# Kernel optimization log

Measured on AMD Instinct MI355X. Metric: run time of the kernel, lower is better.

## Reference

```python
import math
import jax
import jax.numpy as jnp
import numpy as np

B, N, NPOINT, K = 8, 2048, 512, 16
CIN = 64
MLP = [64, 128, 256]
M_W = 8    # PAConv weight-bank size
HID = 16   # scorenet hidden width
GEOM = 10  # 3 rel-xyz + 1 dist + 3 norm + 3 angles


def setup_inputs():
    key = jax.random.key(0)
    ks = jax.random.split(key, 40)
    inp = {}
    inp['xyz'] = jax.random.normal(ks[0], (B, 3, N), jnp.float32)
    inp['norm'] = jax.random.normal(ks[1], (B, 3, N), jnp.float32)
    inp['X_axis'] = jax.random.normal(ks[2], (B, 3, N), jnp.float32)
    inp['Y_axis'] = jax.random.normal(ks[3], (B, 3, N), jnp.float32)
    inp['points'] = jax.random.normal(ks[4], (B, CIN, N), jnp.float32) * 0.5
    cin = CIN
    ki = 5
    for l, cout in enumerate(MLP):
        inp['w1_%d' % l] = jax.random.normal(ks[ki], (HID, GEOM), jnp.float32) / np.sqrt(GEOM); ki += 1
        inp['b1_%d' % l] = jnp.zeros((HID,), jnp.float32)
        inp['w2_%d' % l] = jax.random.normal(ks[ki], (M_W, HID), jnp.float32) / np.sqrt(HID); ki += 1
        inp['b2_%d' % l] = jnp.zeros((M_W,), jnp.float32)
        inp['bank_%d' % l] = jax.random.normal(ks[ki], (M_W, cin, cout), jnp.float32) / np.sqrt(cin); ki += 1
        if l < len(MLP) - 1:
            inp['gamma_%d' % l] = jnp.ones((cout,), jnp.float32)
            inp['beta_%d' % l] = jnp.zeros((cout,), jnp.float32)
        cin = cout
    return inp


def _group(t, idx):
    # t: (B, C, N), idx: (B, ...) int -> (B, C, ...)
    return jax.vmap(lambda p, i: p[:, i])(t, idx)


def _fps(xyz_t, npoint):
    # xyz_t: (B, N, 3) -> (B, npoint) int32; standard iterative FPS starting at index 0
    b, n, _ = xyz_t.shape
    def body(i, c):
        idxs, dists, far = c
        idxs = idxs.at[:, i].set(far)
        centroid = jnp.take_along_axis(xyz_t, far[:, None, None], axis=1)  # (B,1,3)
        d = jnp.sum((xyz_t - centroid) ** 2, axis=-1)
        dists = jnp.minimum(dists, d)
        return idxs, dists, jnp.argmax(dists, axis=-1).astype(jnp.int32)
    idxs = jnp.zeros((b, npoint), jnp.int32)
    dists = jnp.full((b, n), 1e10, xyz_t.dtype)
    far = jnp.zeros((b,), jnp.int32)
    idxs, _, _ = jax.lax.fori_loop(0, npoint, body, (idxs, dists, far))
    return idxs


def _sqdist(a, b):
    # a: (B, P, 3), b: (B, N, 3) -> (B, P, N)
    return (jnp.sum(a ** 2, -1)[:, :, None] + jnp.sum(b ** 2, -1)[:, None, :]
            - 2.0 * jnp.einsum('bpc,bnc->bpn', a, b))


def _angles(gxyz, gn, gX, gY):
    # all (B, 3, P, K) -> (B, 3, P, K); normalized angles to z(norm)/x/y frame axes
    nn = jnp.linalg.norm(gxyz, axis=1)
    def ang(v):
        c = jnp.sum(gxyz * v, axis=1) / (nn * jnp.linalg.norm(v, axis=1) + 1e-8)
        return jnp.arccos(jnp.clip(c, -1.0, 1.0)) / math.pi
    return jnp.stack([ang(gn), ang(gX), ang(gY)], axis=1)


def _paconv(geom, feats, w1, b1, w2, b2, bank, gamma=None, beta=None, act=True):
    # ScoreNet over geometric channels -> softmax scores over M weight matrices
    h = jax.nn.relu(jnp.einsum('hg,bgpk->bhpk', w1, geom) + b1[None, :, None, None])
    s = jax.nn.softmax(jnp.einsum('mh,bhpk->bmpk', w2, h) + b2[None, :, None, None], axis=1)
    out = jnp.einsum('bcpk,mco,bmpk->bopk', feats, bank, s)
    if gamma is not None:
        mu = out.mean(axis=(0, 2, 3), keepdims=True)
        var = out.var(axis=(0, 2, 3), keepdims=True)
        out = (out - mu) / jnp.sqrt(var + 1e-5) * gamma[None, :, None, None] + beta[None, :, None, None]
    return jax.nn.relu(out) if act else out


def reference(xyz, norm, X_axis, Y_axis, points,
              w1_0, b1_0, w2_0, b2_0, bank_0, gamma_0, beta_0,
              w1_1, b1_1, w2_1, b2_1, bank_1, gamma_1, beta_1,
              w1_2, b1_2, w2_2, b2_2, bank_2):
    xyz_t = jnp.transpose(xyz, (0, 2, 1))           # (B,N,3)
    fidx = _fps(xyz_t, NPOINT)                      # (B,NPOINT)
    new_xyz = _group(xyz, fidx)                     # (B,3,NPOINT)
    sq = _sqdist(jnp.transpose(new_xyz, (0, 2, 1)), xyz_t)  # (B,NPOINT,N)
    idx = jax.lax.top_k(-sq, K)[1]                  # (B,NPOINT,K) ascending distance
    grouped_xyz = _group(xyz, idx) - new_xyz[:, :, :, None]  # (B,3,NPOINT,K)
    dist = jnp.sqrt(jnp.sum(grouped_xyz ** 2, axis=1) + 1e-10)  # (B,NPOINT,K)
    dmin = dist.min(axis=2, keepdims=True)
    dist = (dist - dmin) / (dist.max(axis=2, keepdims=True) - dmin + 1e-10)
    new_points = _group(points, idx)                # (B,CIN,NPOINT,K)
    grouped_norm = _group(norm, idx)
    grouped_X = _group(X_axis, idx)
    grouped_Y = _group(Y_axis, idx)
    grouped_angles = _angles(grouped_xyz, grouped_norm, grouped_X, grouped_Y)
    new_norm = grouped_norm[:, :, :, 0]
    new_X = grouped_X[:, :, :, 0]
    new_Y = grouped_Y[:, :, :, 0]
    geom = jnp.concatenate([grouped_xyz, dist[:, None], grouped_norm, grouped_angles], axis=1)  # (B,10,NPOINT,K)
    new_points = _paconv(geom, new_points, w1_0, b1_0, w2_0, b2_0, bank_0, gamma_0, beta_0, act=True)
    new_points = _paconv(geom, new_points, w1_1, b1_1, w2_1, b2_1, bank_1, gamma_1, beta_1, act=True)
    new_points = _paconv(geom, new_points, w1_2, b1_2, w2_2, b2_2, bank_2, None, None, act=False)
    new_points = jnp.max(new_points, axis=3)        # (B,MLP[-1],NPOINT)
    return (new_xyz, new_norm, new_X, new_Y, new_points)
```

## Files before the change

### kernel.cpp

```cpp
#include <hip/hip_runtime.h>
#include <math.h>

#define NBATCH 8
#define NPTS   2048
#define NPOINT 512
#define KNB    16
#define NROWS  (NBATCH*NPOINT*KNB)

typedef unsigned short ushort_t;
typedef unsigned int   uint_t;
typedef unsigned long long ull_t;
typedef __attribute__((ext_vector_type(8))) short  short8;
typedef __attribute__((ext_vector_type(4))) float  f32x4;

#define B0_OFF 0
#define B1_OFF 32768
#define B2_OFF 98304
#define BT_TOT 360448

#define LDS_BARRIER() asm volatile("s_waitcnt lgkmcnt(0)\n\ts_barrier" ::: "memory")

__device__ __align__(16) int      g_fidx[NBATCH * NPOINT];
__device__ __align__(16) int      g_knn [NROWS];
__device__ __align__(16) float    g_sums[1024];
__device__ __align__(16) float    g_pT  [NBATCH * NPTS * 64];
__device__ __align__(16) float    g_S   [(size_t)3 * NROWS * 8];
__device__ __align__(16) float    g_act1[(size_t)NROWS * 64];
__device__ __align__(16) float    g_act2[(size_t)NROWS * 128];
__device__ __align__(16) ushort_t g_bankF[BT_TOT];

__device__ __forceinline__ ushort_t f2bf(float f) {
    uint_t u = __float_as_uint(f);
    return (ushort_t)((u + 0x7FFFu + ((u >> 16) & 1u)) >> 16);
}

template<int CTRL>
__device__ __forceinline__ ull_t dpp_u64(ull_t k) {
    int lo = (int)(uint_t)k;
    int hi = (int)(uint_t)(k >> 32);
    int slo = __builtin_amdgcn_update_dpp(0, lo, CTRL, 0xF, 0xF, true);
    int shi = __builtin_amdgcn_update_dpp(0, hi, CTRL, 0xF, 0xF, true);
    return ((ull_t)(uint_t)shi << 32) | (uint_t)slo;
}

__device__ __forceinline__ ull_t dpp_max_u64(ull_t key) {
    { ull_t s = dpp_u64<0x111>(key); if (s > key) key = s; }
    { ull_t s = dpp_u64<0x112>(key); if (s > key) key = s; }
    { ull_t s = dpp_u64<0x114>(key); if (s > key) key = s; }
    { ull_t s = dpp_u64<0x118>(key); if (s > key) key = s; }
    { ull_t s = dpp_u64<0x142>(key); if (s > key) key = s; }
    { ull_t s = dpp_u64<0x143>(key); if (s > key) key = s; }
    return key;
}

template<int COUT>
__device__ __forceinline__ void bank_frag(const float* __restrict__ bank,
                                          ushort_t* __restrict__ dst, int e) {
    const int j = e & 7;
    const int lane = (e >> 3) & 63;
    const int rem = e >> 9;
    constexpr int NTL = COUT / 16;
    const int nt = rem % NTL;
    const int kc = rem / NTL;
    const int q = lane >> 4, nlo = lane & 15;
    const int k = kc * 32 + q * 8 + j;
    const int n = nt * 16 + nlo;
    dst[e] = f2bf(bank[(size_t)k * COUT + n]);
}

__global__ __launch_bounds__(512) void front_kernel(const float* __restrict__ xyz,
                                                    const float* __restrict__ points,
                                                    const float* __restrict__ bank0,
                                                    const float* __restrict__ bank1,
                                                    const float* __restrict__ bank2) {
    __shared__ float smem[3 * NPTS];
    __shared__ ull_t s_key[2][8];
    const int bid = blockIdx.x;
    const int t = threadIdx.x;

    if (bid >= NBATCH) {
        if (bid < NBATCH + 256) {
            float (*tile)[65] = reinterpret_cast<float(*)[65]>(smem);
            const int blk = bid - NBATCH;
            const int b = blk >> 5;
            const int n0 = (blk & 31) * 64;
            const int lane = t & 63, q = t >> 6;
            #pragma unroll
            for (int i = 0; i < 8; ++i) {
                int c = q * 8 + i;
                tile[c][lane] = points[(b * 64 + c) * NPTS + n0 + lane];
            }
            __syncthreads();
            #pragma unroll
            for (int i = 0; i < 8; ++i) {
                int n = q * 8 + i;
                g_pT[(size_t)(b * NPTS + n0 + n) * 64 + lane] = tile[lane][n];
            }
        } else if (bid == NBATCH + 256) {
            g_sums[t] = 0.0f;
            g_sums[512 + t] = 0.0f;
        } else {
            const int e = (bid - (NBATCH + 257)) * 512 + t;
            if (e < 32768) {
                bank_frag<64>(bank0, g_bankF + B0_OFF, e);
            } else if (e < 98304) {
                bank_frag<128>(bank1, g_bankF + B1_OFF, e - 32768);
            } else {
                bank_frag<256>(bank2, g_bankF + B2_OFF, e - 98304);
            }
        }
        return;
    }

    {
        #pragma clang fp contract(off)
        const int b = bid;
        const int lane = t & 63, w8 = t >> 6;
        const float* xb = xyz + b * 3 * NPTS;
        float* s_x = smem;
        float* s_y = smem + NPTS;
        float* s_z = smem + 2 * NPTS;
        float x[4], y[4], z[4], d[4];
        #pragma unroll
        for (int j = 0; j < 4; ++j) {
            int p = j * 512 + t;
            float vx = xb[p], vy = xb[NPTS + p], vz = xb[2*NPTS + p];
            x[j] = vx; y[j] = vy; z[j] = vz;
            s_x[p] = vx; s_y[p] = vy; s_z[p] = vz;
            d[j] = 1e10f;
        }
        __syncthreads();
        int far = 0;
        for (int i = 0; i < NPOINT; ++i) {
            if (t == 0) g_fidx[b * NPOINT + i] = far;
            float cx = s_x[far], cy = s_y[far], cz = s_z[far];
            float best = -1.0f; int bi = 0;
            #pragma unroll
            for (int j = 0; j < 4; ++j) {
                float dx = x[j] - cx;
                float dy = y[j] - cy;
                float dz = z[j] - cz;
                float dd = dx*dx + dy*dy;
                dd = dd + dz*dz;
                float dn = fminf(d[j], dd);
                d[j] = dn;
                if (dn > best) { best = dn; bi = j * 512 + t; }
            }
            ull_t key = (((ull_t)__float_as_uint(best)) << 32) | (uint_t)(~bi);
            key = dpp_max_u64(key);
            uint_t wlo = (uint_t)__builtin_amdgcn_readlane((int)(uint_t)key, 63);
            uint_t whi = (uint_t)__builtin_amdgcn_readlane((int)(uint_t)(key >> 32), 63);
            if (lane == 0) s_key[i & 1][w8] = ((ull_t)whi << 32) | wlo;
            __syncthreads();
            const ull_t* kb = s_key[i & 1];
            ull_t k0 = kb[0], k1 = kb[1], k2 = kb[2], k3 = kb[3];
            ull_t k4 = kb[4], k5 = kb[5], k6 = kb[6], k7 = kb[7];
            if (k1 > k0) k0 = k1;
            if (k3 > k2) k2 = k3;
            if (k5 > k4) k4 = k5;
            if (k7 > k6) k6 = k7;
            if (k2 > k0) k0 = k2;
            if (k6 > k4) k4 = k6;
            if (k4 > k0) k0 = k4;
            far = (int)(~(uint_t)k0) & (NPTS - 1);
        }
    }
}

__global__ __launch_bounds__(256) void knn_score_kernel(
    const float* __restrict__ xyz, const float* __restrict__ nrm,
    const float* __restrict__ Xa, const float* __restrict__ Ya,
    const float* __restrict__ w1_0, const float* __restrict__ b1_0,
    const float* __restrict__ w2_0, const float* __restrict__ b2_0,
    const float* __restrict__ w1_1, const float* __restrict__ b1_1,
    const float* __restrict__ w2_1, const float* __restrict__ b2_1,
    const float* __restrict__ w1_2, const float* __restrict__ b1_2,
    const float* __restrict__ w2_2, const float* __restrict__ b2_2) {
    __shared__ float w1s[3][16][10];
    __shared__ float b1s[3][16];
    __shared__ float w2s[3][8][16];
    __shared__ float b2s[3][8];
    const int t = threadIdx.x;
    {
        const float* w1p[3] = {w1_0, w1_1, w1_2};
        const float* b1p[3] = {b1_0, b1_1, b1_2};
        const float* w2p[3] = {w2_0, w2_1, w2_2};
        const float* b2p[3] = {b2_0, b2_1, b2_2};
        #pragma unroll
        for (int l = 0; l < 3; ++l) {
            if (t < 160) w1s[l][t / 10][t % 10] = w1p[l][t];
            if (t < 16)  b1s[l][t] = b1p[l][t];
            if (t < 128) w2s[l][t / 16][t % 16] = w2p[l][t];
            if (t < 8)   b2s[l][t] = b2p[l][t];
        }
    }
    __syncthreads();

    const int wave = blockIdx.x * 4 + (t >> 6);
    const int lane = t & 63;
    const int b = wave >> 9;
    const float* xb = xyz + b * 3 * NPTS;
    const int fi = g_fidx[wave] & (NPTS - 1);
    int nmine = 0;

    {
        #pragma clang fp contract(off)
        float ax = xb[fi];
        float ay = xb[NPTS + fi];
        float az = xb[2*NPTS + fi];
        float sa = ax*ax + ay*ay; sa = sa + az*az;
        float d[32];
        #pragma unroll
        for (int j = 0; j < 32; ++j) {
            int pp = j * 64 + lane;
            float bx = xb[pp];
            float by = xb[NPTS + pp];
            float bz = xb[2*NPTS + pp];
            float sb = bx*bx + by*by; sb = sb + bz*bz;
            float dot = ax*bx + ay*by; dot = dot + az*bz;
            float t1 = sa + sb;
            float t2 = 2.0f * dot;
            d[j] = t1 - t2;
        }
        for (int r = 0; r < KNB; ++r) {
            float best = 1e30f; int bi = 0x7fffffff;
            #pragma unroll
            for (int j = 0; j < 32; ++j) {
                if (d[j] < best) { best = d[j]; bi = j * 64 + lane; }
            }
            uint_t ub = __float_as_uint(best);
            ub = (ub & 0x80000000u) ? ~ub : (ub | 0x80000000u);
            ull_t key = ((ull_t)(~ub) << 32) | (uint_t)(~bi);
            key = dpp_max_u64(key);
            uint_t wlo = (uint_t)__builtin_amdgcn_readlane((int)(uint_t)key, 63);
            bi = (int)(~wlo) & (NPTS - 1);
            if (lane == 0) g_knn[wave * KNB + r] = bi;
            if (lane == r) nmine = bi;
            int rl = bi & 63, rs = bi >> 6;
            if (lane == rl) {
                #pragma unroll
                for (int j = 0; j < 32; ++j) if (j == rs) d[j] = 1e30f;
            }
        }
    }

    if (lane < 16) {
        const int row = wave * KNB + lane;
        const int n = nmine & (NPTS - 1);
        const float* nb = nrm + b * 3 * NPTS;
        const float* Xb = Xa  + b * 3 * NPTS;
        const float* Yb = Ya  + b * 3 * NPTS;
        float gx, gy, gz, sq, draw, nnv;
        {
            #pragma clang fp contract(off)
            gx = xb[n]        - xb[fi];
            gy = xb[NPTS + n] - xb[NPTS + fi];
            gz = xb[2*NPTS+n] - xb[2*NPTS+fi];
            sq = gx*gx + gy*gy;
            sq = sq + gz*gz;
            draw = sqrtf(sq + 1e-10f);
            nnv = sqrtf(sq);
        }
        float dmin = draw, dmax = draw;
        #pragma unroll
        for (int m = 1; m < 16; m <<= 1) {
            dmin = fminf(dmin, __shfl_xor(dmin, m, 16));
            dmax = fmaxf(dmax, __shfl_xor(dmax, m, 16));
        }
        float dist;
        {
            #pragma clang fp contract(off)
            dist = (draw - dmin) / ((dmax - dmin) + 1e-10f);
        }
        float nx = nb[n], ny = nb[NPTS+n], nz = nb[2*NPTS+n];
        float Xx = Xb[n], Xy = Xb[NPTS+n], Xz = Xb[2*NPTS+n];
        float Yx = Yb[n], Yy = Yb[NPTS+n], Yz = Yb[2*NPTS+n];
        float g[10];
        g[0]=gx; g[1]=gy; g[2]=gz; g[3]=dist; g[4]=nx; g[5]=ny; g[6]=nz;
        {
            float vs[3][3] = {{nx,ny,nz},{Xx,Xy,Xz},{Yx,Yy,Yz}};
            #pragma unroll
            for (int a = 0; a < 3; ++a) {
                float vx=vs[a][0], vy=vs[a][1], vz=vs[a][2];
                float dot, nv;
                {
                    #pragma clang fp contract(off)
                    dot = gx*vx + gy*vy; dot = dot + gz*vz;
                    float s2 = vx*vx + vy*vy; s2 = s2 + vz*vz;
                    nv = sqrtf(s2);
                }
                float cc = dot / (nnv * nv + 1e-8f);
                cc = fminf(1.0f, fmaxf(-1.0f, cc));
                g[7+a] = acosf(cc) / 3.14159274101257324f;
            }
        }
        #pragma unroll
        for (int l = 0; l < 3; ++l) {
            float h[16];
            #pragma unroll
            for (int i = 0; i < 16; ++i) {
                float a = b1s[l][i];
                #pragma unroll
                for (int j = 0; j < 10; ++j) a += w1s[l][i][j] * g[j];
                h[i] = fmaxf(a, 0.0f);
            }
            float e[8]; float mx = -1e30f;
            #pragma unroll
            for (int m = 0; m < 8; ++m) {
                float a = b2s[l][m];
                #pragma unroll
                for (int j = 0; j < 16; ++j) a += w2s[l][m][j] * h[j];
                e[m] = a; mx = fmaxf(mx, a);
            }
            float sum = 0.0f;
            #pragma unroll
            for (int m = 0; m < 8; ++m) { e[m] = expf(e[m] - mx); sum += e[m]; }
            #pragma unroll
            for (int m = 0; m < 8; ++m)
                g_S[(size_t)l * NROWS * 8 + (size_t)row * 8 + m] = e[m] / sum;
        }
    }
}

template<int LAYER, int CIN, int COUT>
__global__ __launch_bounds__(256) void gemm_kernel(const float* __restrict__ gamma,
                                                   const float* __restrict__ beta,
                                                   float* __restrict__ dout,
                                                   const float* __restrict__ xyz,
                                                   const float* __restrict__ nrm,
                                                   const float* __restrict__ Xa,
                                                   const float* __restrict__ Ya) {
    if constexpr (LAYER == 0) {
        if (blockIdx.x >= 1024) {
            const int g = (blockIdx.x - 1024) * 256 + threadIdx.x;
            const int b = g / NPOINT, p = g % NPOINT;
            const int fi = g_fidx[g] & (NPTS - 1);
            const int n0 = g_knn[g * KNB] & (NPTS - 1);
            #pragma unroll
            for (int a = 0; a < 3; ++a) {
                dout[            (b*3 + a) * NPOINT + p] = xyz[(b*3 + a) * NPTS + fi];
                dout[12288 +     (b*3 + a) * NPOINT + p] = nrm[(b*3 + a) * NPTS + n0];
                dout[24576 +     (b*3 + a) * NPOINT + p] = Xa [(b*3 + a) * NPTS + n0];
                dout[36864 +     (b*3 + a) * NPOINT + p] = Ya [(b*3 + a) * NPTS + n0];
            }
            return;
        }
    }

    const float* __restrict__ A = (LAYER == 0) ? g_pT : (LAYER == 1) ? g_act1 : g_act2;
    float* __restrict__ O = (LAYER == 0) ? g_act1 : (LAYER == 1) ? g_act2 : dout;
    constexpr int NTT = COUT / 16;
    constexpr int NTW = NTT / 4;
    constexpr int CCM = CIN / 32;
    constexpr int BOFF = (LAYER == 0) ? B0_OFF : (LAYER == 1) ? B1_OFF : B2_OFF;
    __shared__ ushort_t As[2][64][36];
    __shared__ float s_scale[(LAYER >= 1) ? CIN : 1];
    __shared__ float s_shift[(LAYER >= 1) ? CIN : 1];
    __shared__ float s_rs[(LAYER < 2) ? COUT : 1];
    __shared__ float s_rss[(LAYER < 2) ? COUT : 1];

    const int t = threadIdx.x;
    const int lane = t & 63, w = t >> 6;
    const int q = lane >> 4, nlo = lane & 15;
    const int row0 = blockIdx.x * 64;
    const int arow_i = t >> 2, acg = t & 3;

    if constexpr (LAYER >= 1) {
        const float* sb = (LAYER == 1) ? g_sums : (g_sums + 256);
        if (t < CIN) {
            float mu  = sb[t] * (1.0f / 65536.0f);
            float var = sb[CIN + t] * (1.0f / 65536.0f) - mu * mu;
            var = fmaxf(var, 0.0f);
            float sc = gamma[t] / sqrtf(var + 1e-5f);
            s_scale[t] = sc;
            s_shift[t] = beta[t] - mu * sc;
        }
        __syncthreads();
    }

    size_t arow;
    if (LAYER == 0) {
        const int row = row0 + arow_i;
        const int b = row >> 13;
        const int n = g_knn[row] & (NPTS - 1);
        arow = (size_t)(b * NPTS + n) * 64;
    } else {
        arow = (size_t)(row0 + arow_i) * CIN;
    }
    const float* Sbase = g_S + (size_t)LAYER * NROWS * 8 + (size_t)(row0 + arow_i) * 8;

    float svv[8];
    #pragma unroll
    for (int m = 0; m < 8; ++m) svv[m] = Sbase[m];

    f32x4 acc[4][NTW];
    #pragma unroll
    for (int mi = 0; mi < 4; ++mi)
        #pragma unroll
        for (int ni = 0; ni < NTW; ++ni) acc[mi][ni] = (f32x4){0.f, 0.f, 0.f, 0.f};

    const ushort_t* fbase = g_bankF + BOFF + lane * 8;

    union FragU { uint4 u4; uint2 u2[2]; short8 s; };
    FragU B[2][NTW];
    #pragma unroll
    for (int ni = 0; ni < NTW; ++ni)
        B[0][ni].u4 = *reinterpret_cast<const uint4*>(fbase + (size_t)(w * NTW + ni) * 512);

    float vraw[8], vnext[8];
    {
        const float* ap = A + arow + acg * 8;
        float4 fa = *reinterpret_cast<const float4*>(ap);
        float4 fb = *reinterpret_cast<const float4*>(ap + 4);
        vraw[0]=fa.x; vraw[1]=fa.y; vraw[2]=fa.z; vraw[3]=fa.w;
        vraw[4]=fb.x; vraw[5]=fb.y; vraw[6]=fb.z; vraw[7]=fb.w;
    }

    int par = 0;
    for (int cc = 0; cc < CCM; ++cc) {
        float v[8];
        #pragma unroll
        for (int j = 0; j < 8; ++j) {
            if constexpr (LAYER >= 1) {
                const int c = cc * 32 + acg * 8 + j;
                v[j] = fmaxf(vraw[j] * s_scale[c] + s_shift[c], 0.f);
            } else {
                v[j] = vraw[j];
            }
        }
        #pragma unroll
        for (int m = 0; m < 8; ++m) {
            {
                const float sv = svv[m];
                uint_t* dst = reinterpret_cast<uint_t*>(&As[par][arow_i][acg * 8]);
                #pragma unroll
                for (int j = 0; j < 8; j += 2)
                    dst[j >> 1] = (uint_t)f2bf(sv * v[j]) | ((uint_t)f2bf(sv * v[j+1]) << 16);
            }
            if (m == 0) {
                const int ccn = (cc + 1 < CCM) ? cc + 1 : cc;
                const float* ap = A + arow + ccn * 32 + acg * 8;
                float4 fa = *reinterpret_cast<const float4*>(ap);
                float4 fb = *reinterpret_cast<const float4*>(ap + 4);
                vnext[0]=fa.x; vnext[1]=fa.y; vnext[2]=fa.z; vnext[3]=fa.w;
                vnext[4]=fb.x; vnext[5]=fb.y; vnext[6]=fb.z; vnext[7]=fb.w;
            }
            {
                const int kcn = (m < 7) ? ((m + 1) * CCM + cc)
                                        : ((cc + 1 < CCM) ? (cc + 1) : 0);
                #pragma unroll
                for (int ni = 0; ni < NTW; ++ni)
                    B[(m + 1) & 1][ni].u4 = *reinterpret_cast<const uint4*>(
                        fbase + (size_t)(kcn * NTT + w * NTW + ni) * 512);
            }
            LDS_BARRIER();
            FragU af[4];
            #pragma unroll
            for (int mi = 0; mi < 4; ++mi) {
                af[mi].u2[0] = *reinterpret_cast<const uint2*>(&As[par][mi*16 + nlo][q*8]);
                af[mi].u2[1] = *reinterpret_cast<const uint2*>(&As[par][mi*16 + nlo][q*8 + 4]);
            }
            #pragma unroll
            for (int ni = 0; ni < NTW; ++ni)
                #pragma unroll
                for (int mi = 0; mi < 4; ++mi)
                    acc[mi][ni] = __builtin_amdgcn_mfma_f32_16x16x32_bf16(
                        af[mi].s, B[m & 1][ni].s, acc[mi][ni], 0, 0, 0);
            par ^= 1;
        }
        #pragma unroll
        for (int j = 0; j < 8; ++j) vraw[j] = vnext[j];
    }

    if constexpr (LAYER == 2) {
        const int bp0 = row0 >> 4;
        #pragma unroll
        for (int mi = 0; mi < 4; ++mi) {
            const int bp = bp0 + mi;
            const int b = bp >> 9, p = bp & 511;
            #pragma unroll
            for (int ni = 0; ni < NTW; ++ni) {
                float mv = fmaxf(fmaxf(acc[mi][ni][0], acc[mi][ni][1]),
                                 fmaxf(acc[mi][ni][2], acc[mi][ni][3]));
                mv = fmaxf(mv, __shfl_xor(mv, 16));
                mv = fmaxf(mv, __shfl_xor(mv, 32));
                if (lane < 16) {
                    const int col = w * 64 + ni * 16 + nlo;
                    O[(size_t)(b * 256 + col) * NPOINT + p] = mv;
                }
            }
        }
    } else {
        #pragma unroll
        for (int mi = 0; mi < 4; ++mi)
            #pragma unroll
            for (int ni = 0; ni < NTW; ++ni)
                #pragma unroll
                for (int r2 = 0; r2 < 4; ++r2)
                    O[(size_t)(row0 + mi*16 + q*4 + r2) * COUT + w*NTW*16 + ni*16 + nlo] = acc[mi][ni][r2];
        #pragma unroll
        for (int ni = 0; ni < NTW; ++ni) {
            float s = 0.f, ss = 0.f;
            #pragma unroll
            for (int mi = 0; mi < 4; ++mi) {
                #pragma unroll
                for (int r2 = 0; r2 < 4; ++r2) {
                    float x = acc[mi][ni][r2];
                    s += x; ss += x * x;
                }
            }
            s  += __shfl_xor(s, 16);  s  += __shfl_xor(s, 32);
            ss += __shfl_xor(ss, 16); ss += __shfl_xor(ss, 32);
            if (q == 0) {
                const int c = w * NTW * 16 + ni * 16 + nlo;
                s_rs[c] = s;
                s_rss[c] = ss;
            }
        }
        __syncthreads();
        if (t < COUT) {
            float* sb = (LAYER == 0) ? g_sums : (g_sums + 256);
            atomicAdd(&sb[t], s_rs[t]);
            atomicAdd(&sb[COUT + t], s_rss[t]);
        }
    }
}

extern "C" void kernel_launch(void* const* d_in, const int* in_sizes, int n_in,
                              void* d_out, int out_size, void* d_ws, size_t ws_size,
                              hipStream_t stream) {
    const float* xyz    = (const float*)d_in[0];
    const float* nrm    = (const float*)d_in[1];
    const float* Xa     = (const float*)d_in[2];
    const float* Ya     = (const float*)d_in[3];
    const float* points = (const float*)d_in[4];
    const float* w1_0 = (const float*)d_in[5];  const float* b1_0 = (const float*)d_in[6];
    const float* w2_0 = (const float*)d_in[7];  const float* b2_0 = (const float*)d_in[8];
    const float* bank0 = (const float*)d_in[9];
    const float* g0 = (const float*)d_in[10];   const float* be0 = (const float*)d_in[11];
    const float* w1_1 = (const float*)d_in[12]; const float* b1_1 = (const float*)d_in[13];
    const float* w2_1 = (const float*)d_in[14]; const float* b2_1 = (const float*)d_in[15];
    const float* bank1 = (const float*)d_in[16];
    const float* g1 = (const float*)d_in[17];   const float* be1 = (const float*)d_in[18];
    const float* w1_2 = (const float*)d_in[19]; const float* b1_2 = (const float*)d_in[20];
    const float* w2_2 = (const float*)d_in[21]; const float* b2_2 = (const float*)d_in[22];
    const float* bank2 = (const float*)d_in[23];
    float* out = (float*)d_out;
    (void)d_ws; (void)ws_size; (void)in_sizes; (void)n_in; (void)out_size;

    front_kernel<<<969, 512, 0, stream>>>(xyz, points, bank0, bank1, bank2);
    knn_score_kernel<<<1024, 256, 0, stream>>>(xyz, nrm, Xa, Ya,
                                               w1_0, b1_0, w2_0, b2_0,
                                               w1_1, b1_1, w2_1, b2_1,
                                               w1_2, b1_2, w2_2, b2_2);
    gemm_kernel<0, 64, 64><<<1040, 256, 0, stream>>>(nullptr, nullptr, out, xyz, nrm, Xa, Ya);
    gemm_kernel<1, 64, 128><<<1024, 256, 0, stream>>>(g0, be0, nullptr, nullptr, nullptr, nullptr, nullptr);
    gemm_kernel<2, 128, 256><<<1024, 256, 0, stream>>>(g1, be1, out + 49152, nullptr, nullptr, nullptr, nullptr);
}
```

Baseline: 507.5 us.

## Shrink FPS block to 4 waves and reduce argmax via 32-bit DPP max

```diff
diff --git a/kernel.cpp b/kernel.cpp
--- a/kernel.cpp
+++ b/kernel.cpp
@@ -51,6 +51,21 @@
     { ull_t s = dpp_u64<0x142>(key); if (s > key) key = s; }
     { ull_t s = dpp_u64<0x143>(key); if (s > key) key = s; }
     return key;
+}
+
+template<int CTRL>
+__device__ __forceinline__ uint_t dpp_u32(uint_t v) {
+    return (uint_t)__builtin_amdgcn_update_dpp(0, (int)v, CTRL, 0xF, 0xF, true);
+}
+
+__device__ __forceinline__ uint_t dpp_max_u32(uint_t v) {
+    { uint_t s = dpp_u32<0x111>(v); if (s > v) v = s; }
+    { uint_t s = dpp_u32<0x112>(v); if (s > v) v = s; }
+    { uint_t s = dpp_u32<0x114>(v); if (s > v) v = s; }
+    { uint_t s = dpp_u32<0x118>(v); if (s > v) v = s; }
+    { uint_t s = dpp_u32<0x142>(v); if (s > v) v = s; }
+    { uint_t s = dpp_u32<0x143>(v); if (s > v) v = s; }
+    return v;
 }
 
 template<int COUT>
@@ -68,13 +83,13 @@
     dst[e] = f2bf(bank[(size_t)k * COUT + n]);
 }
 
-__global__ __launch_bounds__(512) void front_kernel(const float* __restrict__ xyz,
+__global__ __launch_bounds__(256) void front_kernel(const float* __restrict__ xyz,
                                                     const float* __restrict__ points,
                                                     const float* __restrict__ bank0,
                                                     const float* __restrict__ bank1,
                                                     const float* __restrict__ bank2) {
     __shared__ float smem[3 * NPTS];
-    __shared__ ull_t s_key[2][8];
+    __shared__ ull_t s_key[2][4];
     const int bid = blockIdx.x;
     const int t = threadIdx.x;
 
@@ -86,21 +101,23 @@
             const int n0 = (blk & 31) * 64;
             const int lane = t & 63, q = t >> 6;
             #pragma unroll
-            for (int i = 0; i < 8; ++i) {
-                int c = q * 8 + i;
+            for (int i = 0; i < 16; ++i) {
+                int c = q * 16 + i;
                 tile[c][lane] = points[(b * 64 + c) * NPTS + n0 + lane];
             }
             __syncthreads();
             #pragma unroll
-            for (int i = 0; i < 8; ++i) {
-                int n = q * 8 + i;
+            for (int i = 0; i < 16; ++i) {
+                int n = q * 16 + i;
                 g_pT[(size_t)(b * NPTS + n0 + n) * 64 + lane] = tile[lane][n];
             }
         } else if (bid == NBATCH + 256) {
             g_sums[t] = 0.0f;
+            g_sums[256 + t] = 0.0f;
             g_sums[512 + t] = 0.0f;
+            g_sums[768 + t] = 0.0f;
         } else {
-            const int e = (bid - (NBATCH + 257)) * 512 + t;
+            const int e = (bid - (NBATCH + 257)) * 256 + t;
             if (e < 32768) {
                 bank_frag<64>(bank0, g_bankF + B0_OFF, e);
             } else if (e < 98304) {
@@ -115,28 +132,42 @@
     {
         #pragma clang fp contract(off)
         const int b = bid;
-        const int lane = t & 63, w8 = t >> 6;
+        const int lane = t & 63, w = t >> 6;
         const float* xb = xyz + b * 3 * NPTS;
         float* s_x = smem;
         float* s_y = smem + NPTS;
         float* s_z = smem + 2 * NPTS;
-        float x[4], y[4], z[4], d[4];
-        #pragma unroll
-        for (int j = 0; j < 4; ++j) {
-            int p = j * 512 + t;
-            float vx = xb[p], vy = xb[NPTS + p], vz = xb[2*NPTS + p];
-            x[j] = vx; y[j] = vy; z[j] = vz;
-            s_x[p] = vx; s_y[p] = vy; s_z[p] = vz;
-            d[j] = 1e10f;
+        float x[8], y[8], z[8], d[8];
+        {
+            const float4* xp = reinterpret_cast<const float4*>(xb + t * 8);
+            const float4* yp = reinterpret_cast<const float4*>(xb + NPTS + t * 8);
+            const float4* zp = reinterpret_cast<const float4*>(xb + 2 * NPTS + t * 8);
+            float4 a0 = xp[0], a1 = xp[1];
+            float4 b0 = yp[0], b1 = yp[1];
+            float4 c0 = zp[0], c1 = zp[1];
+            x[0]=a0.x; x[1]=a0.y; x[2]=a0.z; x[3]=a0.w;
+            x[4]=a1.x; x[5]=a1.y; x[6]=a1.z; x[7]=a1.w;
+            y[0]=b0.x; y[1]=b0.y; y[2]=b0.z; y[3]=b0.w;
+            y[4]=b1.x; y[5]=b1.y; y[6]=b1.z; y[7]=b1.w;
+            z[0]=c0.x; z[1]=c0.y; z[2]=c0.z; z[3]=c0.w;
+            z[4]=c1.x; z[5]=c1.y; z[6]=c1.z; z[7]=c1.w;
+            *reinterpret_cast<float4*>(s_x + t * 8)     = a0;
+            *reinterpret_cast<float4*>(s_x + t * 8 + 4) = a1;
+            *reinterpret_cast<float4*>(s_y + t * 8)     = b0;
+            *reinterpret_cast<float4*>(s_y + t * 8 + 4) = b1;
+            *reinterpret_cast<float4*>(s_z + t * 8)     = c0;
+            *reinterpret_cast<float4*>(s_z + t * 8 + 4) = c1;
+            #pragma unroll
+            for (int j = 0; j < 8; ++j) d[j] = 1e10f;
         }
         __syncthreads();
         int far = 0;
         for (int i = 0; i < NPOINT; ++i) {
             if (t == 0) g_fidx[b * NPOINT + i] = far;
             float cx = s_x[far], cy = s_y[far], cz = s_z[far];
-            float best = -1.0f; int bi = 0;
-            #pragma unroll
-            for (int j = 0; j < 4; ++j) {
+            uint_t bb = 0u;
+            #pragma unroll
+            for (int j = 0; j < 8; ++j) {
                 float dx = x[j] - cx;
                 float dy = y[j] - cy;
                 float dz = z[j] - cz;
@@ -144,24 +175,26 @@
                 dd = dd + dz*dz;
                 float dn = fminf(d[j], dd);
                 d[j] = dn;
-                if (dn > best) { best = dn; bi = j * 512 + t; }
-            }
-            ull_t key = (((ull_t)__float_as_uint(best)) << 32) | (uint_t)(~bi);
-            key = dpp_max_u64(key);
-            uint_t wlo = (uint_t)__builtin_amdgcn_readlane((int)(uint_t)key, 63);
-            uint_t whi = (uint_t)__builtin_amdgcn_readlane((int)(uint_t)(key >> 32), 63);
-            if (lane == 0) s_key[i & 1][w8] = ((ull_t)whi << 32) | wlo;
-            __syncthreads();
+                uint_t ub = __float_as_uint(dn);
+                bb = (ub > bb) ? ub : bb;
+            }
+            uint_t wm = dpp_max_u32(bb);
+            uint_t wbits = (uint_t)__builtin_amdgcn_readlane((int)wm, 63);
+            int li = 8;
+            #pragma unroll
+            for (int j = 7; j >= 0; --j)
+                li = (__float_as_uint(d[j]) == wbits) ? j : li;
+            ull_t mk = __ballot(li < 8);
+            int fl = __ffsll((unsigned long long)mk) - 1;
+            int wj = __builtin_amdgcn_readlane(li, fl);
+            int wp = ((w << 6) + fl) * 8 + wj;
+            if (lane == 0) s_key[i & 1][w] = ((ull_t)wbits << 32) | (uint_t)(~wp);
+            LDS_BARRIER();
             const ull_t* kb = s_key[i & 1];
             ull_t k0 = kb[0], k1 = kb[1], k2 = kb[2], k3 = kb[3];
-            ull_t k4 = kb[4], k5 = kb[5], k6 = kb[6], k7 = kb[7];
             if (k1 > k0) k0 = k1;
             if (k3 > k2) k2 = k3;
-            if (k5 > k4) k4 = k5;
-            if (k7 > k6) k6 = k7;
             if (k2 > k0) k0 = k2;
-            if (k6 > k4) k4 = k6;
-            if (k4 > k0) k0 = k4;
             far = (int)(~(uint_t)k0) & (NPTS - 1);
         }
     }
@@ -548,7 +581,7 @@
     float* out = (float*)d_out;
     (void)d_ws; (void)ws_size; (void)in_sizes; (void)n_in; (void)out_size;
 
-    front_kernel<<<969, 512, 0, stream>>>(xyz, points, bank0, bank1, bank2);
+    front_kernel<<<1673, 256, 0, stream>>>(xyz, points, bank0, bank1, bank2);
     knn_score_kernel<<<1024, 256, 0, stream>>>(xyz, nrm, Xa, Ya,
                                                w1_0, b1_0, w2_0, b2_0,
                                                w1_1, b1_1, w2_1, b2_1,
```

Measured after the change: 473.4 us. 6.7% less time.

## Restructure FPS loop: 256 threads, packed-f32 distances, broadcast winner coords via LDS

Applied to the files above, without the earlier changes.

```diff
diff --git a/kernel.cpp b/kernel.cpp
--- a/kernel.cpp
+++ b/kernel.cpp
@@ -12,6 +12,7 @@
 typedef unsigned long long ull_t;
 typedef __attribute__((ext_vector_type(8))) short  short8;
 typedef __attribute__((ext_vector_type(4))) float  f32x4;
+typedef __attribute__((ext_vector_type(2))) float  f32x2;
 
 #define B0_OFF 0
 #define B1_OFF 32768
@@ -32,6 +33,13 @@
 __device__ __forceinline__ ushort_t f2bf(float f) {
     uint_t u = __float_as_uint(f);
     return (ushort_t)((u + 0x7FFFu + ((u >> 16) & 1u)) >> 16);
+}
+
+__device__ __forceinline__ f32x2 pk_add(f32x2 a, f32x2 b) {
+    f32x2 r; asm("v_pk_add_f32 %0, %1, %2" : "=v"(r) : "v"(a), "v"(b)); return r;
+}
+__device__ __forceinline__ f32x2 pk_mul(f32x2 a, f32x2 b) {
+    f32x2 r; asm("v_pk_mul_f32 %0, %1, %2" : "=v"(r) : "v"(a), "v"(b)); return r;
 }
 
 template<int CTRL>
@@ -68,13 +76,13 @@
     dst[e] = f2bf(bank[(size_t)k * COUT + n]);
 }
 
-__global__ __launch_bounds__(512) void front_kernel(const float* __restrict__ xyz,
+__global__ __launch_bounds__(256) void front_kernel(const float* __restrict__ xyz,
                                                     const float* __restrict__ points,
                                                     const float* __restrict__ bank0,
                                                     const float* __restrict__ bank1,
                                                     const float* __restrict__ bank2) {
     __shared__ float smem[3 * NPTS];
-    __shared__ ull_t s_key[2][8];
+    __shared__ uint4 s_slot[2][4];
     const int bid = blockIdx.x;
     const int t = threadIdx.x;
 
@@ -86,21 +94,23 @@
             const int n0 = (blk & 31) * 64;
             const int lane = t & 63, q = t >> 6;
             #pragma unroll
-            for (int i = 0; i < 8; ++i) {
-                int c = q * 8 + i;
+            for (int i = 0; i < 16; ++i) {
+                int c = q * 16 + i;
                 tile[c][lane] = points[(b * 64 + c) * NPTS + n0 + lane];
             }
             __syncthreads();
             #pragma unroll
-            for (int i = 0; i < 8; ++i) {
-                int n = q * 8 + i;
+            for (int i = 0; i < 16; ++i) {
+                int n = q * 16 + i;
                 g_pT[(size_t)(b * NPTS + n0 + n) * 64 + lane] = tile[lane][n];
             }
         } else if (bid == NBATCH + 256) {
             g_sums[t] = 0.0f;
+            g_sums[256 + t] = 0.0f;
             g_sums[512 + t] = 0.0f;
+            g_sums[768 + t] = 0.0f;
         } else {
-            const int e = (bid - (NBATCH + 257)) * 512 + t;
+            const int e = (bid - (NBATCH + 257)) * 256 + t;
             if (e < 32768) {
                 bank_frag<64>(bank0, g_bankF + B0_OFF, e);
             } else if (e < 98304) {
@@ -115,54 +125,94 @@
     {
         #pragma clang fp contract(off)
         const int b = bid;
-        const int lane = t & 63, w8 = t >> 6;
+        const int w = t >> 6;
         const float* xb = xyz + b * 3 * NPTS;
-        float* s_x = smem;
-        float* s_y = smem + NPTS;
-        float* s_z = smem + 2 * NPTS;
-        float x[4], y[4], z[4], d[4];
-        #pragma unroll
-        for (int j = 0; j < 4; ++j) {
-            int p = j * 512 + t;
-            float vx = xb[p], vy = xb[NPTS + p], vz = xb[2*NPTS + p];
-            x[j] = vx; y[j] = vy; z[j] = vz;
-            s_x[p] = vx; s_y[p] = vy; s_z[p] = vz;
-            d[j] = 1e10f;
-        }
-        __syncthreads();
-        int far = 0;
-        for (int i = 0; i < NPOINT; ++i) {
-            if (t == 0) g_fidx[b * NPOINT + i] = far;
-            float cx = s_x[far], cy = s_y[far], cz = s_z[far];
-            float best = -1.0f; int bi = 0;
-            #pragma unroll
-            for (int j = 0; j < 4; ++j) {
-                float dx = x[j] - cx;
-                float dy = y[j] - cy;
-                float dz = z[j] - cz;
-                float dd = dx*dx + dy*dy;
-                dd = dd + dz*dz;
-                float dn = fminf(d[j], dd);
-                d[j] = dn;
-                if (dn > best) { best = dn; bi = j * 512 + t; }
-            }
-            ull_t key = (((ull_t)__float_as_uint(best)) << 32) | (uint_t)(~bi);
+        f32x2 xp[4], yp[4], zp[4];
+        float d[8];
+        {
+            const float4* xq = reinterpret_cast<const float4*>(xb + t * 8);
+            const float4* yq = reinterpret_cast<const float4*>(xb + NPTS + t * 8);
+            const float4* zq = reinterpret_cast<const float4*>(xb + 2 * NPTS + t * 8);
+            float4 a0 = xq[0], a1 = xq[1];
+            float4 b0 = yq[0], b1 = yq[1];
+            float4 c0 = zq[0], c1 = zq[1];
+            xp[0] = (f32x2){a0.x, a0.y}; xp[1] = (f32x2){a0.z, a0.w};
+            xp[2] = (f32x2){a1.x, a1.y}; xp[3] = (f32x2){a1.z, a1.w};
+            yp[0] = (f32x2){b0.x, b0.y}; yp[1] = (f32x2){b0.z, b0.w};
+            yp[2] = (f32x2){b1.x, b1.y}; yp[3] = (f32x2){b1.z, b1.w};
+            zp[0] = (f32x2){c0.x, c0.y}; zp[1] = (f32x2){c0.z, c0.w};
+            zp[2] = (f32x2){c1.x, c1.y}; zp[3] = (f32x2){c1.z, c1.w};
+            #pragma unroll
+            for (int j = 0; j < 8; ++j) d[j] = 1e10f;
+        }
+        float cx = xb[0], cy = xb[NPTS], cz = xb[2 * NPTS];
+        if (t == 0) g_fidx[b * NPOINT] = 0;
+
+        for (int i = 0; i < NPOINT - 1; ++i) {
+            const float ncx = -cx, ncy = -cy, ncz = -cz;
+            const f32x2 ncxp = (f32x2){ncx, ncx};
+            const f32x2 ncyp = (f32x2){ncy, ncy};
+            const f32x2 nczp = (f32x2){ncz, ncz};
+            #pragma unroll
+            for (int a = 0; a < 4; ++a) {
+                f32x2 dx = pk_add(xp[a], ncxp);
+                f32x2 dy = pk_add(yp[a], ncyp);
+                f32x2 dz = pk_add(zp[a], nczp);
+                f32x2 px = pk_mul(dx, dx);
+                f32x2 py = pk_mul(dy, dy);
+                f32x2 s  = pk_add(px, py);
+                f32x2 pz = pk_mul(dz, dz);
+                s = pk_add(s, pz);
+                d[2*a]   = fminf(d[2*a],   s[0]);
+                d[2*a+1] = fminf(d[2*a+1], s[1]);
+            }
+            float bb = fmaxf(fmaxf(fmaxf(d[0], d[1]), fmaxf(d[2], d[3])),
+                             fmaxf(fmaxf(d[4], d[5]), fmaxf(d[6], d[7])));
+            const uint_t lb = __float_as_uint(bb);
+            int li = 7;
+            #pragma unroll
+            for (int j = 6; j >= 0; --j)
+                li = (__float_as_uint(d[j]) == lb) ? j : li;
+            ull_t key = ((ull_t)lb << 32) | (uint_t)(~(t * 8 + li));
             key = dpp_max_u64(key);
-            uint_t wlo = (uint_t)__builtin_amdgcn_readlane((int)(uint_t)key, 63);
-            uint_t whi = (uint_t)__builtin_amdgcn_readlane((int)(uint_t)(key >> 32), 63);
-            if (lane == 0) s_key[i & 1][w8] = ((ull_t)whi << 32) | wlo;
-            __syncthreads();
-            const ull_t* kb = s_key[i & 1];
-            ull_t k0 = kb[0], k1 = kb[1], k2 = kb[2], k3 = kb[3];
-            ull_t k4 = kb[4], k5 = kb[5], k6 = kb[6], k7 = kb[7];
-            if (k1 > k0) k0 = k1;
-            if (k3 > k2) k2 = k3;
-            if (k5 > k4) k4 = k5;
-            if (k7 > k6) k6 = k7;
-            if (k2 > k0) k0 = k2;
-            if (k6 > k4) k4 = k6;
-            if (k4 > k0) k0 = k4;
-            far = (int)(~(uint_t)k0) & (NPTS - 1);
+            const uint_t klo = (uint_t)__builtin_amdgcn_readlane((int)(uint_t)key, 63);
+            const uint_t khi = (uint_t)__builtin_amdgcn_readlane((int)(uint_t)(key >> 32), 63);
+            const int wp = (int)(~klo) & (NPTS - 1);
+            if (t == (wp >> 3)) {
+                const int jw = wp & 7;
+                float cxc = xp[0][0], cyc = yp[0][0], czc = zp[0][0];
+                #pragma unroll
+                for (int j = 1; j < 8; ++j) {
+                    const bool m = (jw == j);
+                    cxc = m ? xp[j >> 1][j & 1] : cxc;
+                    cyc = m ? yp[j >> 1][j & 1] : cyc;
+                    czc = m ? zp[j >> 1][j & 1] : czc;
+                }
+                uint4 sl;
+                sl.x = khi;
+                sl.y = __float_as_uint(cxc);
+                sl.z = __float_as_uint(cyc);
+                sl.w = __float_as_uint(czc);
+                s_slot[i & 1][w] = sl;
+            }
+            LDS_BARRIER();
+            const uint4 q0 = s_slot[i & 1][0];
+            const uint4 q1 = s_slot[i & 1][1];
+            const uint4 q2 = s_slot[i & 1][2];
+            const uint4 q3 = s_slot[i & 1][3];
+            const bool v01 = q1.x > q0.x;
+            const uint4 A_ = v01 ? q1 : q0;
+            const int  i01 = v01 ? 1 : 0;
+            const bool v23 = q3.x > q2.x;
+            const uint4 B_ = v23 ? q3 : q2;
+            const int  i23 = v23 ? 3 : 2;
+            const bool vab = B_.x > A_.x;
+            const uint4 C_ = vab ? B_ : A_;
+            const int  wv  = vab ? i23 : i01;
+            cx = __uint_as_float(C_.y);
+            cy = __uint_as_float(C_.z);
+            cz = __uint_as_float(C_.w);
+            if (w == wv && t == (wp >> 3)) g_fidx[b * NPOINT + i + 1] = wp;
         }
     }
 }
@@ -548,7 +598,7 @@
     float* out = (float*)d_out;
     (void)d_ws; (void)ws_size; (void)in_sizes; (void)n_in; (void)out_size;
 
-    front_kernel<<<969, 512, 0, stream>>>(xyz, points, bank0, bank1, bank2);
+    front_kernel<<<1673, 256, 0, stream>>>(xyz, points, bank0, bank1, bank2);
     knn_score_kernel<<<1024, 256, 0, stream>>>(xyz, nrm, Xa, Ya,
                                                w1_0, b1_0, w2_0, b2_0,
                                                w1_1, b1_1, w2_1, b2_1,
```

Measured after the change: 538.1 us. 6.0% more time.
